# Kernel tuning notes

Measured on AMD Instinct MI355X. Metric: run time of the kernel, lower is better.

The kernel has to match this reference:

```python
import jax, jax.numpy as jnp
import numpy as np

N_NODES = 100000
N_EDGES = 1600000


def gcn_conv(x, src, dst, w, W, b, n_nodes):
    # PyG GCNConv: linear -> add self-loops (weight 1) -> symmetric norm -> scatter-add -> bias
    h = x @ W  # [N, out]
    loop = jnp.arange(n_nodes, dtype=src.dtype)
    s = jnp.concatenate([src, loop])
    d = jnp.concatenate([dst, loop])
    ew = jnp.concatenate([w, jnp.ones((n_nodes,), dtype=w.dtype)])
    deg = jax.ops.segment_sum(ew, d, num_segments=n_nodes)  # weighted in-degree (incl. self-loop)
    dis = jnp.where(deg > 0, jax.lax.rsqrt(deg), 0.0)
    norm = dis[s] * ew * dis[d]  # [E+N]
    msgs = norm[:, None] * h[s]  # gather source features, scale per edge
    out = jax.ops.segment_sum(msgs, d, num_segments=n_nodes)  # scatter-add at destinations
    return out + b


def setup_inputs() -> dict:
    key = jax.random.key(0)
    ks = jax.random.split(key, 6)
    x = jax.random.normal(ks[0], (N_NODES, 128), dtype=jnp.float32)
    edge_index = jax.random.randint(ks[1], (2, N_EDGES), 0, N_NODES, dtype=jnp.int32)
    edge_weight = jax.random.uniform(ks[2], (N_EDGES,), dtype=jnp.float32)
    W1 = jax.random.normal(ks[3], (128, 64), dtype=jnp.float32) * (1.0 / np.sqrt(128))
    b1 = jnp.zeros((64,), dtype=jnp.float32)
    W2 = jax.random.normal(ks[4], (64, 16), dtype=jnp.float32) * (1.0 / np.sqrt(64))
    b2 = jnp.zeros((16,), dtype=jnp.float32)
    return {"x": x, "edge_index": edge_index, "edge_weight": edge_weight,
            "W1": W1, "b1": b1, "W2": W2, "b2": b2}


def reference(x, edge_index, edge_weight, W1, b1, W2, b2):
    src, dst = edge_index[0], edge_index[1]
    x_emb = gcn_conv(x, src, dst, edge_weight, W1, b1, N_NODES)
    h = jax.nn.relu(x_emb)  # dropout is identity in eval mode
    out = gcn_conv(h, src, dst, edge_weight, W2, b2, N_NODES)
    return (out, x_emb)
```

## Files before the change

kernel.cpp:

```cpp
#include <hip/hip_runtime.h>

#define NN 100000
#define NE 1600000
#define BSH 7
#define BSZ 128
#define NBKT 782
#define CAP 2560
#define NPB 256
#define EPB 6250

typedef unsigned short u16;
typedef unsigned int   u32;
typedef unsigned long long u64;
typedef __attribute__((ext_vector_type(8))) __bf16 bf16x8;
typedef __attribute__((ext_vector_type(4))) float  f32x4;
typedef __attribute__((ext_vector_type(4))) u32    u32x4;

__device__ __forceinline__ float bf2f(u16 u) {
    union { u32 i; float f; } v; v.i = ((u32)u) << 16; return v.f;
}
__device__ __forceinline__ u16 f2bf(float f) {
    union { float f; u32 i; } v; v.f = f;
    u32 u = v.i;
    u += 0x7FFFu + ((u >> 16) & 1);
    return (u16)(u >> 16);
}
__device__ __forceinline__ float bfLO(u32 p) { return __uint_as_float(p << 16); }
__device__ __forceinline__ float bfHI(u32 p) { return __uint_as_float(p & 0xffff0000u); }

__global__ __launch_bounds__(256) void k_wpack(const float* __restrict__ W1,
                                               const float* __restrict__ W2,
                                               bf16x8* __restrict__ wp1,
                                               bf16x8* __restrict__ wp2,
                                               int* __restrict__ cursor,
                                               int* __restrict__ gctr) {
    int t = threadIdx.x;
    #pragma unroll
    for (int s = 0; s < 4; ++s) {
        int idx = s * 256 + t;
        int q = idx >> 6, l = idx & 63;
        int kb = q >> 2, ct = q & 3;
        int k0 = kb * 32 + ((l >> 4) * 8);
        int c  = ct * 16 + (l & 15);
        bf16x8 v;
        #pragma unroll
        for (int i = 0; i < 8; ++i) v[i] = (__bf16)W1[(k0 + i) * 64 + c];
        wp1[idx] = v;
    }
    if (t < 128) {
        int q = t >> 6, l = t & 63;
        int k0 = q * 32 + ((l >> 4) * 8);
        int c  = l & 15;
        bf16x8 v;
        #pragma unroll
        for (int i = 0; i < 8; ++i) v[i] = (__bf16)W2[(k0 + i) * 16 + c];
        wp2[t] = v;
    }
    for (int i = t; i < NBKT; i += 256) cursor[i] = i * CAP;
    if (t == 0) *gctr = 0;
}

__global__ __launch_bounds__(256) void k_part(const int* __restrict__ src,
                                              const int* __restrict__ dst,
                                              const float* __restrict__ w,
                                              int* __restrict__ cursor,
                                              uint2* __restrict__ rec) {
    __shared__ int cnt[NBKT];
    __shared__ int base[NBKT];
    int tid = threadIdx.x;
    for (int i = tid; i < NBKT; i += 256) cnt[i] = 0;
    __syncthreads();
    int e0 = blockIdx.x * EPB;
    for (int j = tid; j < EPB; j += 256)
        atomicAdd(&cnt[dst[e0 + j] >> BSH], 1);
    __syncthreads();
    for (int i = tid; i < NBKT; i += 256) {
        int c = cnt[i];
        base[i] = c ? atomicAdd(&cursor[i], c) : 0;
    }
    __syncthreads();
    for (int i = tid; i < NBKT; i += 256) cnt[i] = 0;
    __syncthreads();
    for (int j = tid; j < EPB; j += 256) {
        int e  = e0 + j;
        int d  = dst[e];
        int bk = d >> BSH;
        int slot = base[bk] + atomicAdd(&cnt[bk], 1);
        rec[slot] = make_uint2(__float_as_uint(w[e]),
                               ((u32)src[e] << BSH) | (u32)(d & (BSZ - 1)));
    }
}

__global__ __launch_bounds__(256) void k_build(const int* __restrict__ cursor,
                                               const uint2* __restrict__ rec,
                                               uint2* __restrict__ rec2,
                                               float* __restrict__ dis,
                                               int2* __restrict__ rowinfo,
                                               int* __restrict__ gctr) {
    __shared__ float dw[BSZ];
    __shared__ int   cnt[BSZ];
    __shared__ int   base[BSZ];
    __shared__ int   scn[BSZ];
    __shared__ float disl[BSZ];
    __shared__ int   sh_gbase;
    int b = blockIdx.x, tid = threadIdx.x;
    int s = b * CAP;
    int total = cursor[b] - s;
    if (tid < BSZ) { dw[tid] = 1.0f; cnt[tid] = 0; }
    if (tid == 0) sh_gbase = atomicAdd(gctr, total);
    __syncthreads();
    for (int j = tid; j < total; j += 256) {
        uint2 r = rec[s + j];
        int dl = r.y & (BSZ - 1);
        atomicAdd(&cnt[dl], 1);
        atomicAdd(&dw[dl], __uint_as_float(r.x));
    }
    __syncthreads();
    if (tid < BSZ) scn[tid] = cnt[tid];
    __syncthreads();
    #pragma unroll
    for (int off = 1; off < BSZ; off <<= 1) {
        int add = (tid < BSZ && tid >= off) ? scn[tid - off] : 0;
        __syncthreads();
        if (tid < BSZ) scn[tid] += add;
        __syncthreads();
    }
    int gbase = sh_gbase;
    if (tid < BSZ) {
        int node = b * BSZ + tid;
        base[tid] = (tid == 0) ? 0 : scn[tid - 1];
        float d = rsqrtf(dw[tid]);
        disl[tid] = d;
        if (node < NN) {
            dis[node] = d;
            rowinfo[node] = make_int2(gbase + base[tid], gbase + base[tid] + cnt[tid]);
        }
        cnt[tid] = 0;
    }
    __syncthreads();
    for (int j = tid; j < total; j += 256) {
        uint2 r = rec[s + j];
        int dl = r.y & (BSZ - 1);
        int pos = gbase + base[dl] + atomicAdd(&cnt[dl], 1);
        rec2[pos] = make_uint2(__float_as_uint(__uint_as_float(r.x) * disl[dl]),
                               r.y >> BSH);
    }
}

__global__ __launch_bounds__(256) void k_gemm1(const float* __restrict__ x,
                                               const bf16x8* __restrict__ wp1,
                                               const float* __restrict__ dis,
                                               u16* __restrict__ h1b) {
    int tid  = threadIdx.x;
    int lane = tid & 63;
    int wave = tid >> 6;
    int r0   = blockIdx.x * 64 + wave * 16;

    bf16x8 bfrag[16];
    #pragma unroll
    for (int q = 0; q < 16; ++q) bfrag[q] = wp1[q * 64 + lane];

    int  arow = r0 + (lane & 15);
    bool aok  = arow < NN;
    const float* xrow = x + (size_t)arow * 128 + ((lane >> 4) * 8);

    f32x4 acc0 = {0,0,0,0}, acc1 = {0,0,0,0}, acc2 = {0,0,0,0}, acc3 = {0,0,0,0};
    #pragma unroll
    for (int kb = 0; kb < 4; ++kb) {
        f32x4 xlo = {0,0,0,0}, xhi = {0,0,0,0};
        if (aok) {
            xlo = *(const f32x4*)(xrow + kb * 32);
            xhi = *(const f32x4*)(xrow + kb * 32 + 4);
        }
        bf16x8 a;
        a[0] = (__bf16)xlo[0]; a[1] = (__bf16)xlo[1]; a[2] = (__bf16)xlo[2]; a[3] = (__bf16)xlo[3];
        a[4] = (__bf16)xhi[0]; a[5] = (__bf16)xhi[1]; a[6] = (__bf16)xhi[2]; a[7] = (__bf16)xhi[3];
        acc0 = __builtin_amdgcn_mfma_f32_16x16x32_bf16(a, bfrag[kb * 4 + 0], acc0, 0, 0, 0);
        acc1 = __builtin_amdgcn_mfma_f32_16x16x32_bf16(a, bfrag[kb * 4 + 1], acc1, 0, 0, 0);
        acc2 = __builtin_amdgcn_mfma_f32_16x16x32_bf16(a, bfrag[kb * 4 + 2], acc2, 0, 0, 0);
        acc3 = __builtin_amdgcn_mfma_f32_16x16x32_bf16(a, bfrag[kb * 4 + 3], acc3, 0, 0, 0);
    }

    int rbase = r0 + (lane >> 4) * 4;
    int cbase = lane & 15;
    #pragma unroll
    for (int reg = 0; reg < 4; ++reg) {
        int row = rbase + reg;
        if (row < NN) {
            float d = dis[row];
            u16* hp = h1b + (size_t)row * 64 + cbase;
            hp[0]  = f2bf(acc0[reg] * d);
            hp[16] = f2bf(acc1[reg] * d);
            hp[32] = f2bf(acc2[reg] * d);
            hp[48] = f2bf(acc3[reg] * d);
        }
    }
}

#define ACC8(hv, nrm) { \
    a0 = fmaf(nrm, bfLO(hv.x), a0); a1 = fmaf(nrm, bfHI(hv.x), a1); \
    a2 = fmaf(nrm, bfLO(hv.y), a2); a3 = fmaf(nrm, bfHI(hv.y), a3); \
    a4 = fmaf(nrm, bfLO(hv.z), a4); a5 = fmaf(nrm, bfHI(hv.z), a5); \
    a6 = fmaf(nrm, bfLO(hv.w), a6); a7 = fmaf(nrm, bfHI(hv.w), a7); }

__device__ __forceinline__ u64 nt_load_u64(const uint2* p) {
    return __builtin_nontemporal_load((const u64*)p);
}

__global__ __launch_bounds__(1024) void k_agg1(const int2* __restrict__ rowinfo,
                                               const uint2* __restrict__ rec2,
                                               const u16* __restrict__ h1b,
                                               const float* __restrict__ dis,
                                               const float* __restrict__ b1,
                                               float* __restrict__ xemb) {
    int n    = blockIdx.x * 16 + (threadIdx.x >> 6);
    int lane = threadIdx.x & 63;
    int el   = lane >> 3;
    int f8   = (lane & 7) * 8;
    int2 ri  = rowinfo[n];
    int beg = ri.x, end = ri.y;

    float a0=0,a1=0,a2=0,a3=0,a4=0,a5=0,a6=0,a7=0;

    u64 p0 = 0, p1 = 0;
    if (beg + el < end)     p0 = nt_load_u64(&rec2[beg + el]);
    if (beg + 8 + el < end) p1 = nt_load_u64(&rec2[beg + 8 + el]);

    for (int j = beg; j < end; j += 16) {
        u64 q0 = 0, q1 = 0;
        if (j + 16 + el < end) q0 = nt_load_u64(&rec2[j + 16 + el]);
        if (j + 24 + el < end) q1 = nt_load_u64(&rec2[j + 24 + el]);
        if (j + el < end) {
            u32 srcn = (u32)(p0 >> 32);
            float nrm = __uint_as_float((u32)p0);
            uint4 hv = *(const uint4*)(h1b + (size_t)srcn * 64 + f8);
            ACC8(hv, nrm);
        }
        if (j + 8 + el < end) {
            u32 srcn = (u32)(p1 >> 32);
            float nrm = __uint_as_float((u32)p1);
            uint4 hv = *(const uint4*)(h1b + (size_t)srcn * 64 + f8);
            ACC8(hv, nrm);
        }
        p0 = q0; p1 = q1;
    }

    #pragma unroll
    for (int m = 8; m <= 32; m <<= 1) {
        a0 += __shfl_xor(a0, m, 64); a1 += __shfl_xor(a1, m, 64);
        a2 += __shfl_xor(a2, m, 64); a3 += __shfl_xor(a3, m, 64);
        a4 += __shfl_xor(a4, m, 64); a5 += __shfl_xor(a5, m, 64);
        a6 += __shfl_xor(a6, m, 64); a7 += __shfl_xor(a7, m, 64);
    }
    if (el == 0) {
        float di = dis[n];
        uint4 hv = *(const uint4*)(h1b + (size_t)n * 64 + f8);
        f32x4 lo, hi;
        lo[0] = fmaf(di, bfLO(hv.x), b1[f8 + 0]) + a0;
        lo[1] = fmaf(di, bfHI(hv.x), b1[f8 + 1]) + a1;
        lo[2] = fmaf(di, bfLO(hv.y), b1[f8 + 2]) + a2;
        lo[3] = fmaf(di, bfHI(hv.y), b1[f8 + 3]) + a3;
        hi[0] = fmaf(di, bfLO(hv.z), b1[f8 + 4]) + a4;
        hi[1] = fmaf(di, bfHI(hv.z), b1[f8 + 5]) + a5;
        hi[2] = fmaf(di, bfLO(hv.w), b1[f8 + 6]) + a6;
        hi[3] = fmaf(di, bfHI(hv.w), b1[f8 + 7]) + a7;
        f32x4* dst0 = (f32x4*)&xemb[(size_t)n * 64 + f8];
        __builtin_nontemporal_store(lo, dst0);
        __builtin_nontemporal_store(hi, dst0 + 1);
    }
}

__global__ __launch_bounds__(256) void k_gemm2(const float* __restrict__ xemb,
                                               const bf16x8* __restrict__ wp2,
                                               const float* __restrict__ dis,
                                               u16* __restrict__ h3b) {
    int tid  = threadIdx.x;
    int lane = tid & 63;
    int wave = tid >> 6;
    int r0   = blockIdx.x * 64 + wave * 16;

    bf16x8 b0 = wp2[lane], b1 = wp2[64 + lane];

    int  arow = r0 + (lane & 15);
    bool aok  = arow < NN;
    const float* xrow = xemb + (size_t)arow * 64 + ((lane >> 4) * 8);

    f32x4 acc = {0,0,0,0};
    #pragma unroll
    for (int kb = 0; kb < 2; ++kb) {
        f32x4 xlo = {0,0,0,0}, xhi = {0,0,0,0};
        if (aok) {
            xlo = *(const f32x4*)(xrow + kb * 32);
            xhi = *(const f32x4*)(xrow + kb * 32 + 4);
        }
        bf16x8 a;
        #pragma unroll
        for (int i = 0; i < 4; ++i) {
            float lo = xlo[i] > 0.f ? xlo[i] : 0.f;
            float hi = xhi[i] > 0.f ? xhi[i] : 0.f;
            a[i]     = (__bf16)lo;
            a[i + 4] = (__bf16)hi;
        }
        acc = __builtin_amdgcn_mfma_f32_16x16x32_bf16(a, kb == 0 ? b0 : b1, acc, 0, 0, 0);
    }

    int rbase = r0 + (lane >> 4) * 4;
    int cbase = lane & 15;
    #pragma unroll
    for (int reg = 0; reg < 4; ++reg) {
        int row = rbase + reg;
        if (row < NN)
            h3b[(size_t)row * 16 + cbase] = f2bf(acc[reg] * dis[row]);
    }
}

__global__ __launch_bounds__(1024) void k_agg2(const int2* __restrict__ rowinfo,
                                               const uint2* __restrict__ rec2,
                                               const u16* __restrict__ h3b,
                                               const float* __restrict__ dis,
                                               const float* __restrict__ b2,
                                               float* __restrict__ out) {
    int n    = blockIdx.x * 16 + (threadIdx.x >> 6);
    int lane = threadIdx.x & 63;
    int el   = lane >> 2;
    int f4   = (lane & 3) * 4;
    int2 ri  = rowinfo[n];
    int beg = ri.x, end = ri.y;

    float a0=0,a1=0,a2=0,a3=0;

    u64 p0 = 0, p1 = 0;
    if (beg + el < end)      p0 = nt_load_u64(&rec2[beg + el]);
    if (beg + 16 + el < end) p1 = nt_load_u64(&rec2[beg + 16 + el]);

    for (int j = beg; j < end; j += 32) {
        u64 q0 = 0, q1 = 0;
        if (j + 32 + el < end) q0 = nt_load_u64(&rec2[j + 32 + el]);
        if (j + 48 + el < end) q1 = nt_load_u64(&rec2[j + 48 + el]);
        if (j + el < end) {
            u32 srcn = (u32)(p0 >> 32);
            float nrm = __uint_as_float((u32)p0);
            uint2 hv = *(const uint2*)(h3b + (size_t)srcn * 16 + f4);
            a0 = fmaf(nrm, bfLO(hv.x), a0); a1 = fmaf(nrm, bfHI(hv.x), a1);
            a2 = fmaf(nrm, bfLO(hv.y), a2); a3 = fmaf(nrm, bfHI(hv.y), a3);
        }
        if (j + 16 + el < end) {
            u32 srcn = (u32)(p1 >> 32);
            float nrm = __uint_as_float((u32)p1);
            uint2 hv = *(const uint2*)(h3b + (size_t)srcn * 16 + f4);
            a0 = fmaf(nrm, bfLO(hv.x), a0); a1 = fmaf(nrm, bfHI(hv.x), a1);
            a2 = fmaf(nrm, bfLO(hv.y), a2); a3 = fmaf(nrm, bfHI(hv.y), a3);
        }
        p0 = q0; p1 = q1;
    }

    #pragma unroll
    for (int m = 4; m <= 32; m <<= 1) {
        a0 += __shfl_xor(a0, m, 64);
        a1 += __shfl_xor(a1, m, 64);
        a2 += __shfl_xor(a2, m, 64);
        a3 += __shfl_xor(a3, m, 64);
    }
    if (lane < 4) {
        float di = dis[n];
        uint2 hv = *(const uint2*)(h3b + (size_t)n * 16 + f4);
        float4 bb = *(const float4*)&b2[f4];
        float4 r;
        r.x = fmaf(di, bfLO(hv.x), bb.x) + a0;
        r.y = fmaf(di, bfHI(hv.x), bb.y) + a1;
        r.z = fmaf(di, bfLO(hv.y), bb.z) + a2;
        r.w = fmaf(di, bfHI(hv.y), bb.w) + a3;
        *(float4*)&out[(size_t)n * 16 + f4] = r;
    }
}

extern "C" void kernel_launch(void* const* d_in, const int* in_sizes, int n_in,
                              void* d_out, int out_size, void* d_ws, size_t ws_size,
                              hipStream_t stream) {
    const float* x  = (const float*)d_in[0];
    const int*   ei = (const int*)d_in[1];
    const float* w  = (const float*)d_in[2];
    const float* W1 = (const float*)d_in[3];
    const float* b1 = (const float*)d_in[4];
    const float* W2 = (const float*)d_in[5];
    const float* b2 = (const float*)d_in[6];
    const int* src = ei;
    const int* dst = ei + NE;

    float* out2 = (float*)d_out;
    float* xemb = (float*)d_out + NN * 16;

    uint2*  rec_pad = (uint2*)d_ws;
    u16*    h1b     = (u16*)d_ws;
    uint2*  rec2    = rec_pad + (size_t)NBKT * CAP;
    u16*    h3b     = (u16*)(rec2 + NE);
    bf16x8* wp1     = (bf16x8*)(h3b + (size_t)NN * 16);
    bf16x8* wp2     = wp1 + 1024;
    float*  dis     = (float*)(wp2 + 128);
    int2*   rowinfo = (int2*)(dis + NN);
    int*    cursor  = (int*)(rowinfo + NN);
    int*    gctr    = cursor + NBKT;

    k_wpack<<<1,    256, 0, stream>>>(W1, W2, wp1, wp2, cursor, gctr);
    k_part <<<NPB,  256, 0, stream>>>(src, dst, w, cursor, rec_pad);
    k_build<<<NBKT, 256, 0, stream>>>(cursor, rec_pad, rec2, dis, rowinfo, gctr);

    k_gemm1<<<(NN + 63) / 64, 256, 0, stream>>>(x, wp1, dis, h1b);
    k_agg1 <<<NN / 16, 1024, 0, stream>>>(rowinfo, rec2, h1b, dis, b1, xemb);

    k_gemm2<<<(NN + 63) / 64, 256, 0, stream>>>(xemb, wp2, dis, h3b);
    k_agg2 <<<NN / 16, 1024, 0, stream>>>(rowinfo, rec2, h3b, dis, b2, out2);
}
```

Measured before the change: 179.3 us.

## Split layer-1 aggregation into four 16-column chunks with chunk-major features

The first-layer hidden features are stored chunk-major as four 16-column bf16 slabs, and aggregation runs as four passes, one per slab. Each gathered working set (100k nodes x 32 bytes) is small enough to stay in cache, which is meant to cut random-gather DRAM traffic. In exchange the edge list is re-read four times, three extra kernel launches are added, and each gather is only 8 bytes per lane.

```diff
diff --git a/kernel.cpp b/kernel.cpp
--- a/kernel.cpp
+++ b/kernel.cpp
@@ -14,7 +14,6 @@
 typedef unsigned long long u64;
 typedef __attribute__((ext_vector_type(8))) __bf16 bf16x8;
 typedef __attribute__((ext_vector_type(4))) float  f32x4;
-typedef __attribute__((ext_vector_type(4))) u32    u32x4;
 
 __device__ __forceinline__ float bf2f(u16 u) {
     union { u32 i; float f; } v; v.i = ((u32)u) << 16; return v.f;
@@ -27,6 +26,9 @@
 }
 __device__ __forceinline__ float bfLO(u32 p) { return __uint_as_float(p << 16); }
 __device__ __forceinline__ float bfHI(u32 p) { return __uint_as_float(p & 0xffff0000u); }
+__device__ __forceinline__ u64 nt_load_u64(const uint2* p) {
+    return __builtin_nontemporal_load((const u64*)p);
+}
 
 __global__ __launch_bounds__(256) void k_wpack(const float* __restrict__ W1,
                                                const float* __restrict__ W2,
@@ -150,7 +152,7 @@
 __global__ __launch_bounds__(256) void k_gemm1(const float* __restrict__ x,
                                                const bf16x8* __restrict__ wp1,
                                                const float* __restrict__ dis,
-                                               u16* __restrict__ h1b) {
+                                               u16* __restrict__ h1bc) {
     int tid  = threadIdx.x;
     int lane = tid & 63;
     int wave = tid >> 6;
@@ -188,85 +190,72 @@
         int row = rbase + reg;
         if (row < NN) {
             float d = dis[row];
-            u16* hp = h1b + (size_t)row * 64 + cbase;
-            hp[0]  = f2bf(acc0[reg] * d);
-            hp[16] = f2bf(acc1[reg] * d);
-            hp[32] = f2bf(acc2[reg] * d);
-            hp[48] = f2bf(acc3[reg] * d);
-        }
-    }
-}
-
-#define ACC8(hv, nrm) { \
-    a0 = fmaf(nrm, bfLO(hv.x), a0); a1 = fmaf(nrm, bfHI(hv.x), a1); \
-    a2 = fmaf(nrm, bfLO(hv.y), a2); a3 = fmaf(nrm, bfHI(hv.y), a3); \
-    a4 = fmaf(nrm, bfLO(hv.z), a4); a5 = fmaf(nrm, bfHI(hv.z), a5); \
-    a6 = fmaf(nrm, bfLO(hv.w), a6); a7 = fmaf(nrm, bfHI(hv.w), a7); }
-
-__device__ __forceinline__ u64 nt_load_u64(const uint2* p) {
-    return __builtin_nontemporal_load((const u64*)p);
-}
-
-__global__ __launch_bounds__(1024) void k_agg1(const int2* __restrict__ rowinfo,
-                                               const uint2* __restrict__ rec2,
-                                               const u16* __restrict__ h1b,
-                                               const float* __restrict__ dis,
-                                               const float* __restrict__ b1,
-                                               float* __restrict__ xemb) {
+            u16* hp = h1bc + (size_t)row * 16 + cbase;
+            hp[0 * NN * 16] = f2bf(acc0[reg] * d);
+            hp[1 * NN * 16] = f2bf(acc1[reg] * d);
+            hp[2 * NN * 16] = f2bf(acc2[reg] * d);
+            hp[3 * NN * 16] = f2bf(acc3[reg] * d);
+        }
+    }
+}
+
+__global__ __launch_bounds__(1024) void k_agg1p(const int2* __restrict__ rowinfo,
+                                                const uint2* __restrict__ rec2,
+                                                const u16* __restrict__ h1bc,
+                                                const float* __restrict__ dis,
+                                                const float* __restrict__ b1c,
+                                                float* __restrict__ xemb_c) {
     int n    = blockIdx.x * 16 + (threadIdx.x >> 6);
     int lane = threadIdx.x & 63;
-    int el   = lane >> 3;
-    int f8   = (lane & 7) * 8;
+    int el   = lane >> 2;
+    int fi   = (lane & 3) * 4;
     int2 ri  = rowinfo[n];
     int beg = ri.x, end = ri.y;
 
-    float a0=0,a1=0,a2=0,a3=0,a4=0,a5=0,a6=0,a7=0;
+    float a0=0,a1=0,a2=0,a3=0;
 
     u64 p0 = 0, p1 = 0;
-    if (beg + el < end)     p0 = nt_load_u64(&rec2[beg + el]);
-    if (beg + 8 + el < end) p1 = nt_load_u64(&rec2[beg + 8 + el]);
-
-    for (int j = beg; j < end; j += 16) {
+    if (beg + el < end)      p0 = nt_load_u64(&rec2[beg + el]);
+    if (beg + 16 + el < end) p1 = nt_load_u64(&rec2[beg + 16 + el]);
+
+    for (int j = beg; j < end; j += 32) {
         u64 q0 = 0, q1 = 0;
-        if (j + 16 + el < end) q0 = nt_load_u64(&rec2[j + 16 + el]);
-        if (j + 24 + el < end) q1 = nt_load_u64(&rec2[j + 24 + el]);
+        if (j + 32 + el < end) q0 = nt_load_u64(&rec2[j + 32 + el]);
+        if (j + 48 + el < end) q1 = nt_load_u64(&rec2[j + 48 + el]);
         if (j + el < end) {
             u32 srcn = (u32)(p0 >> 32);
             float nrm = __uint_as_float((u32)p0);
-            uint4 hv = *(const uint4*)(h1b + (size_t)srcn * 64 + f8);
-            ACC8(hv, nrm);
-        }
-        if (j + 8 + el < end) {
+            uint2 hv = *(const uint2*)(h1bc + (size_t)srcn * 16 + fi);
+            a0 = fmaf(nrm, bfLO(hv.x), a0); a1 = fmaf(nrm, bfHI(hv.x), a1);
+            a2 = fmaf(nrm, bfLO(hv.y), a2); a3 = fmaf(nrm, bfHI(hv.y), a3);
+        }
+        if (j + 16 + el < end) {
             u32 srcn = (u32)(p1 >> 32);
             float nrm = __uint_as_float((u32)p1);
-            uint4 hv = *(const uint4*)(h1b + (size_t)srcn * 64 + f8);
-            ACC8(hv, nrm);
+            uint2 hv = *(const uint2*)(h1bc + (size_t)srcn * 16 + fi);
+            a0 = fmaf(nrm, bfLO(hv.x), a0); a1 = fmaf(nrm, bfHI(hv.x), a1);
+            a2 = fmaf(nrm, bfLO(hv.y), a2); a3 = fmaf(nrm, bfHI(hv.y), a3);
         }
         p0 = q0; p1 = q1;
     }
 
     #pragma unroll
-    for (int m = 8; m <= 32; m <<= 1) {
-        a0 += __shfl_xor(a0, m, 64); a1 += __shfl_xor(a1, m, 64);
-        a2 += __shfl_xor(a2, m, 64); a3 += __shfl_xor(a3, m, 64);
-        a4 += __shfl_xor(a4, m, 64); a5 += __shfl_xor(a5, m, 64);
-        a6 += __shfl_xor(a6, m, 64); a7 += __shfl_xor(a7, m, 64);
-    }
-    if (el == 0) {
+    for (int m = 4; m <= 32; m <<= 1) {
+        a0 += __shfl_xor(a0, m, 64);
+        a1 += __shfl_xor(a1, m, 64);
+        a2 += __shfl_xor(a2, m, 64);
+        a3 += __shfl_xor(a3, m, 64);
+    }
+    if (lane < 4) {
         float di = dis[n];
-        uint4 hv = *(const uint4*)(h1b + (size_t)n * 64 + f8);
-        f32x4 lo, hi;
-        lo[0] = fmaf(di, bfLO(hv.x), b1[f8 + 0]) + a0;
-        lo[1] = fmaf(di, bfHI(hv.x), b1[f8 + 1]) + a1;
-        lo[2] = fmaf(di, bfLO(hv.y), b1[f8 + 2]) + a2;
-        lo[3] = fmaf(di, bfHI(hv.y), b1[f8 + 3]) + a3;
-        hi[0] = fmaf(di, bfLO(hv.z), b1[f8 + 4]) + a4;
-        hi[1] = fmaf(di, bfHI(hv.z), b1[f8 + 5]) + a5;
-        hi[2] = fmaf(di, bfLO(hv.w), b1[f8 + 6]) + a6;
-        hi[3] = fmaf(di, bfHI(hv.w), b1[f8 + 7]) + a7;
-        f32x4* dst0 = (f32x4*)&xemb[(size_t)n * 64 + f8];
-        __builtin_nontemporal_store(lo, dst0);
-        __builtin_nontemporal_store(hi, dst0 + 1);
+        uint2 hv = *(const uint2*)(h1bc + (size_t)n * 16 + fi);
+        float4 bb = *(const float4*)&b1c[fi];
+        f32x4 r;
+        r[0] = fmaf(di, bfLO(hv.x), bb.x) + a0;
+        r[1] = fmaf(di, bfHI(hv.x), bb.y) + a1;
+        r[2] = fmaf(di, bfLO(hv.y), bb.z) + a2;
+        r[3] = fmaf(di, bfHI(hv.y), bb.w) + a3;
+        __builtin_nontemporal_store(r, (f32x4*)&xemb_c[(size_t)n * 64 + fi]);
     }
 }
 
@@ -391,7 +380,7 @@
     float* xemb = (float*)d_out + NN * 16;
 
     uint2*  rec_pad = (uint2*)d_ws;
-    u16*    h1b     = (u16*)d_ws;
+    u16*    h1bc    = (u16*)d_ws;
     uint2*  rec2    = rec_pad + (size_t)NBKT * CAP;
     u16*    h3b     = (u16*)(rec2 + NE);
     bf16x8* wp1     = (bf16x8*)(h3b + (size_t)NN * 16);
@@ -405,8 +394,11 @@
     k_part <<<NPB,  256, 0, stream>>>(src, dst, w, cursor, rec_pad);
     k_build<<<NBKT, 256, 0, stream>>>(cursor, rec_pad, rec2, dis, rowinfo, gctr);
 
-    k_gemm1<<<(NN + 63) / 64, 256, 0, stream>>>(x, wp1, dis, h1b);
-    k_agg1 <<<NN / 16, 1024, 0, stream>>>(rowinfo, rec2, h1b, dis, b1, xemb);
+    k_gemm1<<<(NN + 63) / 64, 256, 0, stream>>>(x, wp1, dis, h1bc);
+    for (int c = 0; c < 4; ++c)
+        k_agg1p<<<NN / 16, 1024, 0, stream>>>(rowinfo, rec2,
+                                              h1bc + (size_t)c * NN * 16,
+                                              dis, b1 + c * 16, xemb + c * 16);
 
     k_gemm2<<<(NN + 63) / 64, 256, 0, stream>>>(xemb, wp2, dis, h3b);
     k_agg2 <<<NN / 16, 1024, 0, stream>>>(rowinfo, rec2, h3b, dis, b2, out2);
```

Result: slower. 270.7 us (+51.0%).
